# Kernel optimization log

Hardware: AMD Instinct MI355X
Metric: run time of the kernel (lower is better)

## Reference

```python
import jax, jax.numpy as jnp
import numpy as np

M, N, F = 512, 128, 512  # molecules, atoms per molecule, feature dim
HID, OUT = F // 4, 1


def setup_inputs() -> dict:
    key = jax.random.key(0)
    k1, k2, k3 = jax.random.split(key, 3)
    h = jax.random.normal(k1, (M, N, F), dtype=jnp.float32)
    W1 = jax.random.normal(k2, (F, HID), dtype=jnp.float32) * (1.0 / np.sqrt(F))
    b1 = jnp.zeros((HID,), dtype=jnp.float32)
    W2 = jax.random.normal(k3, (HID, OUT), dtype=jnp.float32) * (1.0 / np.sqrt(HID))
    b2 = jnp.zeros((OUT,), dtype=jnp.float32)
    return {"h": h, "W1": W1, "b1": b1, "W2": W2, "b2": b2}


def reference(h, W1, b1, W2, b2):
    # method == 'weighted_summation'
    # gate MLP: Linear -> ReLU -> Linear -> Sigmoid, per atom
    w = jax.nn.sigmoid(jax.nn.relu(h @ W1 + b1) @ W2 + b2)  # [M, N, OUT]
    # per-molecule weighted sum over atoms: mm(w_h.T, h) for each molecule,
    # concatenated along dim 0 -> [M*OUT, F] (OUT=1 -> [M, F])
    out = jnp.einsum('mno,mnf->mof', w, h)  # [M, OUT, F]
    return out.reshape(M * OUT, F)
```

## Files before the change

kernel.cpp:

```cpp
#include <hip/hip_runtime.h>
#include <hip/hip_bf16.h>


typedef unsigned short u16;
typedef unsigned int u32;
typedef __bf16 bf16x8 __attribute__((ext_vector_type(8)));
typedef float f32x4 __attribute__((ext_vector_type(4)));
typedef float f32x2 __attribute__((ext_vector_type(2)));
typedef u32 u32x4 __attribute__((ext_vector_type(4)));

#define M_MOL 512
#define N_ATOM 128
#define F_DIM 512
#define HID_DIM 128
#define ABLK 64
#define NBLK (M_MOL * 2)

static __device__ __forceinline__ u16 f2bf(float x) {
  u32 u = __float_as_uint(x);
  u32 r = (u + 0x7fffu + ((u >> 16) & 1u)) >> 16;
  return (u16)r;
}
static __device__ __forceinline__ bf16x8 pack8(u32x4 a, u32x4 b) {
  u32x4 r;
  r[0] = (a[0] >> 16) | (a[1] & 0xffff0000u);
  r[1] = (a[2] >> 16) | (a[3] & 0xffff0000u);
  r[2] = (b[0] >> 16) | (b[1] & 0xffff0000u);
  r[3] = (b[2] >> 16) | (b[3] & 0xffff0000u);
  return __builtin_bit_cast(bf16x8, r);
}

__global__ __launch_bounds__(256) void transpose_w1(const float* __restrict__ W1,
                                                    u16* __restrict__ W1Tt) {
  __shared__ float tile[64][65];
  const int k0 = blockIdx.x * 64;
  const int n0 = blockIdx.y * 64;
  const int t = threadIdx.x;
  #pragma unroll
  for (int i = 0; i < 16; ++i) {
    const int lin = i * 256 + t;
    const int lr = lin >> 6, lc = lin & 63;
    tile[lc][lr] = W1[(size_t)(k0 + lr) * HID_DIM + (n0 + lc)];
  }
  __syncthreads();
  #pragma unroll
  for (int i = 0; i < 16; ++i) {
    const int lin = i * 256 + t;
    const int wr = lin >> 6, wc = lin & 63;
    const int k = k0 + wc;
    W1Tt[(size_t)(k >> 5) * (HID_DIM * 32) + (size_t)(n0 + wr) * 32 + (k & 31)] =
        f2bf(tile[wr][wc]);
  }
}

__global__ __launch_bounds__(512, 4) void pool_partial(
    const float* __restrict__ h, const u16* __restrict__ W1Tt,
    const float* __restrict__ b1, const float* __restrict__ W2,
    const float* __restrict__ b2, float* __restrict__ part) {
  __shared__ __align__(16) u16 As[ABLK * F_DIM];
  __shared__ float w_s[ABLK];

  const int blk = blockIdx.x;
  const int tid = threadIdx.x;
  const int wv = tid >> 6;
  const int lane = tid & 63;
  const int quad = lane >> 4;
  const int cl = lane & 15;

  u16* AsW = As + wv * (8 * F_DIM);

  {
    const float* hw = h + (size_t)blk * (ABLK * F_DIM) + (size_t)(wv * 8) * F_DIM;
    #pragma unroll
    for (int g = 0; g < 2; ++g) {
      u32x4 lo[4], hi[4];
      #pragma unroll
      for (int i2 = 0; i2 < 4; ++i2) {
        const int i = g * 4 + i2;
        const u32x4* src = (const u32x4*)(hw + (size_t)i * F_DIM) + 2 * lane;
        lo[i2] = src[0];
        hi[i2] = src[1];
      }
      #pragma unroll
      for (int i2 = 0; i2 < 4; ++i2) {
        const int i = g * 4 + i2;
        const int phys = (lane & ~7) | ((lane ^ i) & 7);
        *(bf16x8*)(AsW + i * F_DIM + phys * 8) = pack8(lo[i2], hi[i2]);
      }
    }
  }

  const u16* bg = W1Tt + cl * 32 + quad * 8;

  asm volatile("s_waitcnt lgkmcnt(0)" ::: "memory");
  __builtin_amdgcn_sched_barrier(0);

  f32x4 acc[8];
  #pragma unroll
  for (int t = 0; t < 8; ++t) acc[t] = (f32x4){0.f, 0.f, 0.f, 0.f};

  const u16* aBase = AsW + (cl & 7) * F_DIM;

  #pragma unroll
  for (int ks = 0; ks < 16; ++ks) {
    u32x4 bfr[8];
    #pragma unroll
    for (int t = 0; t < 8; ++t)
      bfr[t] = *(const u32x4*)(bg + (size_t)ks * (HID_DIM * 32) + t * 512);
    const int c = ks * 4 + quad;
    const int aphys = (c & ~7) | ((c ^ cl) & 7);
    bf16x8 afr = *(const bf16x8*)(aBase + aphys * 8);
    #pragma unroll
    for (int t = 0; t < 8; ++t)
      acc[t] = __builtin_amdgcn_mfma_f32_16x16x32_bf16(
          afr, __builtin_bit_cast(bf16x8, bfr[t]), acc[t], 0, 0, 0);
  }

  float psum[4] = {0.f, 0.f, 0.f, 0.f};
  #pragma unroll
  for (int t = 0; t < 8; ++t) {
    const int hid = t * 16 + cl;
    const float b1v = b1[hid];
    const float w2v = W2[hid];
    #pragma unroll
    for (int r = 0; r < 4; ++r) {
      float tv = fmaxf(acc[t][r] + b1v, 0.f);
      psum[r] = fmaf(tv, w2v, psum[r]);
    }
  }
  #pragma unroll
  for (int off = 1; off < 16; off <<= 1)
    #pragma unroll
    for (int r = 0; r < 4; ++r)
      psum[r] += __shfl_xor(psum[r], off, 64);
  if (cl == 0 && quad < 2) {
    const float b2v = b2[0];
    #pragma unroll
    for (int r = 0; r < 4; ++r)
      w_s[wv * 8 + quad * 4 + r] = 1.f / (1.f + __expf(-(psum[r] + b2v)));
  }
  asm volatile("s_waitcnt lgkmcnt(0)" ::: "memory");
  __builtin_amdgcn_sched_barrier(0);

  float facc[8] = {0.f, 0.f, 0.f, 0.f, 0.f, 0.f, 0.f, 0.f};
  #pragma unroll
  for (int i = 0; i < 8; ++i) {
    const float wn = w_s[wv * 8 + i];
    const int phys = (lane & ~7) | ((lane ^ i) & 7);
    bf16x8 hv = *(const bf16x8*)(AsW + i * F_DIM + phys * 8);
    u32x4 uv = __builtin_bit_cast(u32x4, hv);
    #pragma unroll
    for (int j = 0; j < 4; ++j) {
      facc[2 * j]     = fmaf(wn, __uint_as_float(uv[j] << 16), facc[2 * j]);
      facc[2 * j + 1] = fmaf(wn, __uint_as_float(uv[j] & 0xffff0000u), facc[2 * j + 1]);
    }
  }

  float* red = (float*)As;
  __syncthreads();
  #pragma unroll
  for (int j = 0; j < 8; ++j) red[wv * F_DIM + lane * 8 + j] = facc[j];
  __syncthreads();

  {
    const int f = tid;
    float o = 0.f;
    #pragma unroll
    for (int w = 0; w < 8; ++w) o += red[w * F_DIM + f];
    part[(size_t)blk * F_DIM + f] = o;
  }
}

__global__ __launch_bounds__(256) void reduce_out(const float* __restrict__ part,
                                                  float* __restrict__ out) {
  const int m = blockIdx.x;
  const int f = threadIdx.x * 2;
  f32x2 a = *(const f32x2*)(part + (size_t)(2 * m) * F_DIM + f);
  f32x2 b = *(const f32x2*)(part + (size_t)(2 * m + 1) * F_DIM + f);
  f32x2 o;
  o[0] = a[0] + b[0];
  o[1] = a[1] + b[1];
  *(f32x2*)(out + (size_t)m * F_DIM + f) = o;
}

extern "C" void kernel_launch(void* const* d_in, const int* in_sizes, int n_in,
                              void* d_out, int out_size, void* d_ws, size_t ws_size,
                              hipStream_t stream) {
  const float* h  = (const float*)d_in[0];
  const float* W1 = (const float*)d_in[1];
  const float* b1 = (const float*)d_in[2];
  const float* W2 = (const float*)d_in[3];
  const float* b2 = (const float*)d_in[4];
  float* out = (float*)d_out;

  u16* W1Tt = (u16*)d_ws;
  float* part = (float*)((char*)d_ws + (size_t)HID_DIM * F_DIM * sizeof(u16));

  transpose_w1<<<dim3(8, 2), 256, 0, stream>>>(W1, W1Tt);
  pool_partial<<<NBLK, 512, 0, stream>>>(h, W1Tt, b1, W2, b2, part);
  reduce_out<<<M_MOL, 256, 0, stream>>>(part, out);
}
```

Measured before the change: 241.8 us.

## Split fused pool into register-pipelined gate pass and separate weighted-sum pass

Replaces the fused kernel, which staged h through LDS as bf16, with two passes. The gate pass loads A fragments straight from global memory into registers, with software prefetch of the next k-step, and writes per-atom sigmoid weights to a buffer. A second kernel then rereads h in fp32 to form the weighted sum per molecule. This drops the large LDS allocation and its barriers and uses fp32 h in the weighted sum, but reads all of h from memory twice.

```diff
diff --git a/kernel.cpp b/kernel.cpp
--- a/kernel.cpp
+++ b/kernel.cpp
@@ -13,8 +13,6 @@
 #define N_ATOM 128
 #define F_DIM 512
 #define HID_DIM 128
-#define ABLK 64
-#define NBLK (M_MOL * 2)
 
 static __device__ __forceinline__ u16 f2bf(float x) {
   u32 u = __float_as_uint(x);
@@ -53,67 +51,47 @@
   }
 }
 
-__global__ __launch_bounds__(512, 4) void pool_partial(
+__global__ __launch_bounds__(256) void gate_pass(
     const float* __restrict__ h, const u16* __restrict__ W1Tt,
     const float* __restrict__ b1, const float* __restrict__ W2,
-    const float* __restrict__ b2, float* __restrict__ part) {
-  __shared__ __align__(16) u16 As[ABLK * F_DIM];
-  __shared__ float w_s[ABLK];
-
-  const int blk = blockIdx.x;
+    const float* __restrict__ b2, float* __restrict__ wbuf) {
   const int tid = threadIdx.x;
   const int wv = tid >> 6;
   const int lane = tid & 63;
   const int quad = lane >> 4;
   const int cl = lane & 15;
 
-  u16* AsW = As + wv * (8 * F_DIM);
-
-  {
-    const float* hw = h + (size_t)blk * (ABLK * F_DIM) + (size_t)(wv * 8) * F_DIM;
-    #pragma unroll
-    for (int g = 0; g < 2; ++g) {
-      u32x4 lo[4], hi[4];
-      #pragma unroll
-      for (int i2 = 0; i2 < 4; ++i2) {
-        const int i = g * 4 + i2;
-        const u32x4* src = (const u32x4*)(hw + (size_t)i * F_DIM) + 2 * lane;
-        lo[i2] = src[0];
-        hi[i2] = src[1];
-      }
-      #pragma unroll
-      for (int i2 = 0; i2 < 4; ++i2) {
-        const int i = g * 4 + i2;
-        const int phys = (lane & ~7) | ((lane ^ i) & 7);
-        *(bf16x8*)(AsW + i * F_DIM + phys * 8) = pack8(lo[i2], hi[i2]);
-      }
-    }
-  }
-
+  const int row0 = blockIdx.x * 64 + wv * 16;
+  const u32x4* ap = (const u32x4*)(h + (size_t)(row0 + cl) * F_DIM) + quad * 2;
   const u16* bg = W1Tt + cl * 32 + quad * 8;
-
-  asm volatile("s_waitcnt lgkmcnt(0)" ::: "memory");
-  __builtin_amdgcn_sched_barrier(0);
 
   f32x4 acc[8];
   #pragma unroll
   for (int t = 0; t < 8; ++t) acc[t] = (f32x4){0.f, 0.f, 0.f, 0.f};
 
-  const u16* aBase = AsW + (cl & 7) * F_DIM;
+  u32x4 aC0 = ap[0], aC1 = ap[1];
+  u32x4 bC[8];
+  #pragma unroll
+  for (int t = 0; t < 8; ++t) bC[t] = *(const u32x4*)(bg + t * 512);
 
   #pragma unroll
   for (int ks = 0; ks < 16; ++ks) {
-    u32x4 bfr[8];
-    #pragma unroll
-    for (int t = 0; t < 8; ++t)
-      bfr[t] = *(const u32x4*)(bg + (size_t)ks * (HID_DIM * 32) + t * 512);
-    const int c = ks * 4 + quad;
-    const int aphys = (c & ~7) | ((c ^ cl) & 7);
-    bf16x8 afr = *(const bf16x8*)(aBase + aphys * 8);
+    u32x4 aN0, aN1, bN[8];
+    if (ks < 15) {
+      aN0 = ap[(ks + 1) * 8];
+      aN1 = ap[(ks + 1) * 8 + 1];
+      #pragma unroll
+      for (int t = 0; t < 8; ++t)
+        bN[t] = *(const u32x4*)(bg + (size_t)(ks + 1) * (HID_DIM * 32) + t * 512);
+    }
+    bf16x8 afr = pack8(aC0, aC1);
     #pragma unroll
     for (int t = 0; t < 8; ++t)
       acc[t] = __builtin_amdgcn_mfma_f32_16x16x32_bf16(
-          afr, __builtin_bit_cast(bf16x8, bfr[t]), acc[t], 0, 0, 0);
+          afr, __builtin_bit_cast(bf16x8, bC[t]), acc[t], 0, 0, 0);
+    aC0 = aN0; aC1 = aN1;
+    #pragma unroll
+    for (int t = 0; t < 8; ++t) bC[t] = bN[t];
   }
 
   float psum[4] = {0.f, 0.f, 0.f, 0.f};
@@ -133,54 +111,38 @@
     #pragma unroll
     for (int r = 0; r < 4; ++r)
       psum[r] += __shfl_xor(psum[r], off, 64);
-  if (cl == 0 && quad < 2) {
+  if (cl == 0) {
     const float b2v = b2[0];
     #pragma unroll
     for (int r = 0; r < 4; ++r)
-      w_s[wv * 8 + quad * 4 + r] = 1.f / (1.f + __expf(-(psum[r] + b2v)));
-  }
-  asm volatile("s_waitcnt lgkmcnt(0)" ::: "memory");
-  __builtin_amdgcn_sched_barrier(0);
-
-  float facc[8] = {0.f, 0.f, 0.f, 0.f, 0.f, 0.f, 0.f, 0.f};
-  #pragma unroll
-  for (int i = 0; i < 8; ++i) {
-    const float wn = w_s[wv * 8 + i];
-    const int phys = (lane & ~7) | ((lane ^ i) & 7);
-    bf16x8 hv = *(const bf16x8*)(AsW + i * F_DIM + phys * 8);
-    u32x4 uv = __builtin_bit_cast(u32x4, hv);
-    #pragma unroll
-    for (int j = 0; j < 4; ++j) {
-      facc[2 * j]     = fmaf(wn, __uint_as_float(uv[j] << 16), facc[2 * j]);
-      facc[2 * j + 1] = fmaf(wn, __uint_as_float(uv[j] & 0xffff0000u), facc[2 * j + 1]);
-    }
-  }
-
-  float* red = (float*)As;
-  __syncthreads();
-  #pragma unroll
-  for (int j = 0; j < 8; ++j) red[wv * F_DIM + lane * 8 + j] = facc[j];
-  __syncthreads();
-
-  {
-    const int f = tid;
-    float o = 0.f;
-    #pragma unroll
-    for (int w = 0; w < 8; ++w) o += red[w * F_DIM + f];
-    part[(size_t)blk * F_DIM + f] = o;
+      wbuf[row0 + quad * 4 + r] = 1.f / (1.f + __expf(-(psum[r] + b2v)));
   }
 }
 
-__global__ __launch_bounds__(256) void reduce_out(const float* __restrict__ part,
-                                                  float* __restrict__ out) {
+__global__ __launch_bounds__(256) void weight_pass(
+    const float* __restrict__ h, const float* __restrict__ wbuf,
+    float* __restrict__ out) {
   const int m = blockIdx.x;
-  const int f = threadIdx.x * 2;
-  f32x2 a = *(const f32x2*)(part + (size_t)(2 * m) * F_DIM + f);
-  f32x2 b = *(const f32x2*)(part + (size_t)(2 * m + 1) * F_DIM + f);
-  f32x2 o;
-  o[0] = a[0] + b[0];
-  o[1] = a[1] + b[1];
-  *(f32x2*)(out + (size_t)m * F_DIM + f) = o;
+  const int f0 = threadIdx.x * 2;
+  const float* hm = h + (size_t)m * (N_ATOM * F_DIM);
+  const float* wm = wbuf + (size_t)m * N_ATOM;
+
+  float a0 = 0.f, a1 = 0.f;
+  #pragma unroll 2
+  for (int n0 = 0; n0 < N_ATOM; n0 += 8) {
+    f32x2 v[8];
+    #pragma unroll
+    for (int j = 0; j < 8; ++j)
+      v[j] = *(const f32x2*)(hm + (size_t)(n0 + j) * F_DIM + f0);
+    #pragma unroll
+    for (int j = 0; j < 8; ++j) {
+      const float wn = wm[n0 + j];
+      a0 = fmaf(wn, v[j][0], a0);
+      a1 = fmaf(wn, v[j][1], a1);
+    }
+  }
+  f32x2 o; o[0] = a0; o[1] = a1;
+  *(f32x2*)(out + (size_t)m * F_DIM + f0) = o;
 }
 
 extern "C" void kernel_launch(void* const* d_in, const int* in_sizes, int n_in,
@@ -194,9 +156,9 @@
   float* out = (float*)d_out;
 
   u16* W1Tt = (u16*)d_ws;
-  float* part = (float*)((char*)d_ws + (size_t)HID_DIM * F_DIM * sizeof(u16));
+  float* wbuf = (float*)((char*)d_ws + (size_t)HID_DIM * F_DIM * sizeof(u16));
 
   transpose_w1<<<dim3(8, 2), 256, 0, stream>>>(W1, W1Tt);
-  pool_partial<<<NBLK, 512, 0, stream>>>(h, W1Tt, b1, W2, b2, part);
-  reduce_out<<<M_MOL, 256, 0, stream>>>(part, out);
+  gate_pass<<<M_MOL * 2, 256, 0, stream>>>(h, W1Tt, b1, W2, b2, wbuf);
+  weight_pass<<<M_MOL, 256, 0, stream>>>(h, wbuf, out);
 }
```

Measured after the change: 227.5 us. 1.06x faster.
